# Optimization experiments

Hardware: AMD Instinct MI355X
Metric: run time of the kernel (lower is better)

Reference implementation:

```python
import jax, jax.numpy as jnp
import numpy as np

ALPHA = 0.6
K = 4


def gsdnef_conv(x, edge_index, W, b, alpha, K):
    """SpGSDNEFConv: linear transform then K-step graph-signal-denoising diffusion
    h_{k+1} = (x + alpha * A_hat h_k) / (1 + alpha), A_hat = D^-1/2 (A+I) D^-1/2."""
    n = x.shape[0]
    x = x @ W + b  # [N, C_out]
    loop = jnp.arange(n, dtype=edge_index.dtype)
    src = jnp.concatenate([edge_index[0], loop])
    dst = jnp.concatenate([edge_index[1], loop])
    ones = jnp.ones(src.shape, dtype=x.dtype)
    deg = jax.ops.segment_sum(ones, dst, num_segments=n)
    dinv = jax.lax.rsqrt(jnp.maximum(deg, 1e-12))
    norm = dinv[src] * dinv[dst]  # [E+N]
    inv = 1.0 / (1.0 + alpha)
    h = x
    for _ in range(K):
        agg = jax.ops.segment_sum(h[src] * norm[:, None], dst, num_segments=n)
        h = (x + alpha * agg) * inv
    return h


def setup_inputs() -> dict:
    key = jax.random.key(0)
    ks = jax.random.split(key, 16)
    N, E, C_in, H, C_out = 50000, 800000, 256, 128, 64
    x = jax.random.normal(ks[0], (N, C_in), dtype=jnp.float32)
    edge_index = jax.random.randint(ks[1], (2, E), 0, N, dtype=jnp.int64)

    def lin(k, fan_in, fan_out):
        k1, k2 = jax.random.split(k)
        bound = 1.0 / np.sqrt(fan_in)
        W = jax.random.uniform(k1, (fan_in, fan_out), jnp.float32, -bound, bound)
        b = jax.random.uniform(k2, (fan_out,), jnp.float32, -bound, bound)
        return W, b

    Wc1, bc1 = lin(ks[2], C_in, H)
    Wl1, bl1 = lin(ks[3], C_in, H)
    Wc2, bc2 = lin(ks[4], H, H)
    Wl2, bl2 = lin(ks[5], H, H)
    Wc3, bc3 = lin(ks[6], H, C_out)
    Wl3, bl3 = lin(ks[7], H, C_out)
    return dict(x=x, edge_index=edge_index,
                Wc1=Wc1, bc1=bc1, Wl1=Wl1, bl1=bl1,
                Wc2=Wc2, bc2=bc2, Wl2=Wl2, bl2=bl2,
                Wc3=Wc3, bc3=bc3, Wl3=Wl3, bl3=bl3)


def reference(x, edge_index, Wc1, bc1, Wl1, bl1, Wc2, bc2, Wl2, bl2, Wc3, bc3, Wl3, bl3):
    h = jax.nn.elu(gsdnef_conv(x, edge_index, Wc1, bc1, ALPHA, K) + (x @ Wl1 + bl1))
    h = jax.nn.elu(gsdnef_conv(h, edge_index, Wc2, bc2, ALPHA, K) + (h @ Wl2 + bl2))
    h = gsdnef_conv(h, edge_index, Wc3, bc3, ALPHA, K) + (h @ Wl3 + bl3)
    return h
```

## Files before the change

### kernel.cpp

```cpp
#include <hip/hip_runtime.h>
#include <hip/hip_fp16.h>
#include <math.h>

#define ALPHA_C 0.6f

typedef _Float16 f16;
typedef f16 f16x8 __attribute__((ext_vector_type(8)));
typedef float f32x4 __attribute__((ext_vector_type(4)));

__global__ void detect_idx_kernel(const void* __restrict__ ei, int* __restrict__ flag,
                                  int E, int N) {
    int i = blockIdx.x * blockDim.x + threadIdx.x;
    if (i >= E) return;
    long long v = ((const long long*)ei)[i];
    if (v < 0 || v >= (long long)N) *flag = 1;
}

__global__ void convert_idx_kernel(const void* __restrict__ ei, const int* __restrict__ flag,
                                   int* __restrict__ out, int n2e) {
    int i = blockIdx.x * blockDim.x + threadIdx.x;
    if (i >= n2e) return;
    if (*flag == 0)
        out[i] = (int)((const long long*)ei)[i];
    else
        out[i] = ((const int*)ei)[i];
}

__global__ void count_kernel(const int* __restrict__ dst, int* __restrict__ cnt, int E) {
    int i = blockIdx.x * blockDim.x + threadIdx.x;
    if (i < E) atomicAdd(&cnt[dst[i]], 1);
}

__global__ void dinv_kernel(const int* __restrict__ cnt, float* __restrict__ dinv, int N) {
    int i = blockIdx.x * blockDim.x + threadIdx.x;
    if (i < N) dinv[i] = rsqrtf((float)cnt[i] + 1.0f);
}

__global__ void block_reduce_kernel(const int* __restrict__ cnt, int* __restrict__ bsum, int n) {
    __shared__ int s[256];
    int tid = threadIdx.x;
    int i = blockIdx.x * 256 + tid;
    int v = (i < n) ? cnt[i] : 0;
    s[tid] = v;
    __syncthreads();
    for (int o = 128; o > 0; o >>= 1) {
        if (tid < o) s[tid] += s[tid + o];
        __syncthreads();
    }
    if (tid == 0) bsum[blockIdx.x] = s[0];
}

__global__ void scan_top_kernel(int* __restrict__ bsum, int nb) {
    __shared__ int s[1024];
    int tid = threadIdx.x;
    int v = (tid < nb) ? bsum[tid] : 0;
    s[tid] = v;
    __syncthreads();
    for (int o = 1; o < 1024; o <<= 1) {
        int t = (tid >= o) ? s[tid - o] : 0;
        __syncthreads();
        s[tid] += t;
        __syncthreads();
    }
    if (tid < nb) bsum[tid] = s[tid] - v;
}

__global__ void scan_fill_kernel(const int* __restrict__ cnt, const int* __restrict__ bsum,
                                 int* __restrict__ row_off, int n) {
    __shared__ int s[256];
    int tid = threadIdx.x;
    int i = blockIdx.x * 256 + tid;
    int v = (i < n) ? cnt[i] : 0;
    s[tid] = v;
    __syncthreads();
    for (int o = 1; o < 256; o <<= 1) {
        int t = (tid >= o) ? s[tid - o] : 0;
        __syncthreads();
        s[tid] += t;
        __syncthreads();
    }
    int base = bsum[blockIdx.x];
    if (i < n) row_off[i] = base + s[tid] - v;
    if (i == n - 1) row_off[n] = base + s[tid];
}

__global__ void fill_kernel(const int* __restrict__ src, const int* __restrict__ dst,
                            const float* __restrict__ dinv, const int* __restrict__ row_off,
                            int* __restrict__ cursor, unsigned int* __restrict__ csre, int E) {
    int e = blockIdx.x * blockDim.x + threadIdx.x;
    if (e >= E) return;
    int d = dst[e], s = src[e];
    int pos = atomicAdd(&cursor[d], 1);
    int idx = row_off[d] + pos;
    float w = dinv[s] * dinv[d];
    csre[idx] = (unsigned int)s |
                ((unsigned int)__half_as_ushort(__float2half(w)) << 16);
}

__global__ void prep_all_w_kernel(
    const float* __restrict__ Wc1, const float* __restrict__ Wl1,
    const float* __restrict__ Wc2, const float* __restrict__ Wl2,
    const float* __restrict__ Wc3, const float* __restrict__ Wl3,
    f16* __restrict__ w1c, f16* __restrict__ w1l,
    f16* __restrict__ w2c, f16* __restrict__ w2l,
    f16* __restrict__ w3c, f16* __restrict__ w3l) {
    int i = blockIdx.x * blockDim.x + threadIdx.x;
    const float* W; f16* O; int K, Nn, base;
    if      (i <  32768) { W = Wc1; O = w1c; K = 256; Nn = 128; base = i; }
    else if (i <  65536) { W = Wl1; O = w1l; K = 256; Nn = 128; base = i - 32768; }
    else if (i <  81920) { W = Wc2; O = w2c; K = 128; Nn = 128; base = i - 65536; }
    else if (i <  98304) { W = Wl2; O = w2l; K = 128; Nn = 128; base = i - 81920; }
    else if (i < 106496) { W = Wc3; O = w3c; K = 128; Nn = 64;  base = i - 98304; }
    else if (i < 114688) { W = Wl3; O = w3l; K = 128; Nn = 64;  base = i - 106496; }
    else return;
    int k = base / Nn, n = base - k * Nn;
    O[(size_t)n * K + k] = (f16)W[base];
}

template <int K, int NH, int AMODE>
__global__ __launch_bounds__(256) void gemm2_kernel(
    const void* __restrict__ A0v, const void* __restrict__ A1v,
    const f16* __restrict__ WtA, const f16* __restrict__ WtB,
    const float* __restrict__ biasA, const float* __restrict__ biasB,
    f16* __restrict__ CA, f16* __restrict__ CB, int M) {
    constexpr int BM = 64, BK = 64;
    constexpr int NT = 2 * NH / 16;
    constexpr int LDA = BK + 8;
    __shared__ f16 At[BM][LDA];
    __shared__ f16 Wt[2 * NH][LDA];

    int tid = threadIdx.x;
    int wave = tid >> 6, lane = tid & 63;
    int lr = lane & 15, lhi = lane >> 4;
    int m0 = blockIdx.x * BM;

    f32x4 acc[NT];
#pragma unroll
    for (int n = 0; n < NT; ++n) acc[n] = (f32x4){0.f, 0.f, 0.f, 0.f};

    for (int k0 = 0; k0 < K; k0 += BK) {
        for (int c = tid; c < BM * 8; c += 256) {
            int row = c >> 3, kc = (c & 7) << 3;
            f16x8 v;
#pragma unroll
            for (int j = 0; j < 8; ++j) v[j] = (f16)0.f;
            if (m0 + row < M) {
                size_t idx = (size_t)(m0 + row) * K + k0 + kc;
                if constexpr (AMODE == 0) {
                    v = *(const f16x8*)((const f16*)A0v + idx);
                } else if constexpr (AMODE == 1) {
                    float4 a = *(const float4*)((const float*)A0v + idx);
                    float4 b = *(const float4*)((const float*)A0v + idx + 4);
                    v[0] = (f16)a.x; v[1] = (f16)a.y; v[2] = (f16)a.z; v[3] = (f16)a.w;
                    v[4] = (f16)b.x; v[5] = (f16)b.y; v[6] = (f16)b.z; v[7] = (f16)b.w;
                } else {
                    f16x8 u0 = *(const f16x8*)((const f16*)A0v + idx);
                    f16x8 u1 = *(const f16x8*)((const f16*)A1v + idx);
#pragma unroll
                    for (int j = 0; j < 8; ++j) {
                        float t = (float)u0[j] + (float)u1[j];
                        v[j] = (f16)(t > 0.f ? t : expm1f(t));
                    }
                }
            }
            *(f16x8*)&At[row][kc] = v;
        }
        for (int c = tid; c < NH * 8; c += 256) {
            int row = c >> 3, kc = (c & 7) << 3;
            *(f16x8*)&Wt[row][kc]      = *(const f16x8*)(WtA + (size_t)row * K + k0 + kc);
            *(f16x8*)&Wt[NH + row][kc] = *(const f16x8*)(WtB + (size_t)row * K + k0 + kc);
        }
        __syncthreads();
#pragma unroll
        for (int kk = 0; kk < BK; kk += 32) {
            f16x8 a = *(const f16x8*)&At[wave * 16 + lr][kk + lhi * 8];
#pragma unroll
            for (int n = 0; n < NT; ++n) {
                f16x8 b = *(const f16x8*)&Wt[n * 16 + lr][kk + lhi * 8];
                acc[n] = __builtin_amdgcn_mfma_f32_16x16x32_f16(a, b, acc[n], 0, 0, 0);
            }
        }
        __syncthreads();
    }

    int rbase = m0 + wave * 16 + lhi * 4;
#pragma unroll
    for (int n = 0; n < NT; ++n) {
        bool isA = (n < NT / 2);
        int colg = (isA ? n : n - NT / 2) * 16 + lr;
        f16* outp = isA ? CA : CB;
        float bv = (isA ? biasA : biasB)[colg];
#pragma unroll
        for (int r = 0; r < 4; ++r) {
            int row = rbase + r;
            if (row < M) outp[(size_t)row * NH + colg] = (f16)(acc[n][r] + bv);
        }
    }
}

template <int C, bool FINAL>
__global__ __launch_bounds__(256) void diffuse16_kernel(
    const __half* __restrict__ h, const __half* __restrict__ xc,
    const float* __restrict__ dinv, const int* __restrict__ row_off,
    const unsigned int* __restrict__ csre, __half* __restrict__ hout,
    const f16* __restrict__ lin, float* __restrict__ fout, int N) {
    const float inv = 1.0f / (1.0f + ALPHA_C);
    int gid = blockIdx.x * blockDim.x + threadIdx.x;
    int node = gid >> 6;
    if (node >= N) return;
    int lane = threadIdx.x & 63;
    int l = lane & 15, grp = lane >> 4;
    float di = dinv[node];
    float di2 = di * di;
    int e0 = row_off[node], e1 = row_off[node + 1];

    if constexpr (C == 128) {
        float acc[8];
#pragma unroll
        for (int i = 0; i < 8; ++i) acc[i] = 0.f;
        size_t coff = (size_t)l * 8;

        if (grp == 0) {
            float4 rv = *(const float4*)(h + ((size_t)node << 7) + coff);
            const __half2* p = (const __half2*)&rv;
#pragma unroll
            for (int k = 0; k < 4; ++k) {
                float2 f = __half22float2(p[k]);
                acc[2 * k] += di2 * f.x;
                acc[2 * k + 1] += di2 * f.y;
            }
        }
        int e = e0 + grp;
        for (; e + 12 < e1; e += 16) {
            unsigned int ev0 = csre[e], ev1 = csre[e + 4], ev2 = csre[e + 8], ev3 = csre[e + 12];
            float4 r0 = *(const float4*)(h + ((size_t)(ev0 & 0xFFFF) << 7) + coff);
            float4 r1 = *(const float4*)(h + ((size_t)(ev1 & 0xFFFF) << 7) + coff);
            float4 r2 = *(const float4*)(h + ((size_t)(ev2 & 0xFFFF) << 7) + coff);
            float4 r3 = *(const float4*)(h + ((size_t)(ev3 & 0xFFFF) << 7) + coff);
            float w0 = __half2float(__ushort_as_half((unsigned short)(ev0 >> 16)));
            float w1 = __half2float(__ushort_as_half((unsigned short)(ev1 >> 16)));
            float w2 = __half2float(__ushort_as_half((unsigned short)(ev2 >> 16)));
            float w3 = __half2float(__ushort_as_half((unsigned short)(ev3 >> 16)));
            const __half2* p0 = (const __half2*)&r0;
            const __half2* p1 = (const __half2*)&r1;
            const __half2* p2 = (const __half2*)&r2;
            const __half2* p3 = (const __half2*)&r3;
#pragma unroll
            for (int k = 0; k < 4; ++k) {
                float2 f0 = __half22float2(p0[k]);
                float2 f1 = __half22float2(p1[k]);
                float2 f2 = __half22float2(p2[k]);
                float2 f3 = __half22float2(p3[k]);
                acc[2 * k]     += w0 * f0.x + w1 * f1.x + w2 * f2.x + w3 * f3.x;
                acc[2 * k + 1] += w0 * f0.y + w1 * f1.y + w2 * f2.y + w3 * f3.y;
            }
        }
        for (; e < e1; e += 4) {
            unsigned int ev0 = csre[e];
            float4 r0 = *(const float4*)(h + ((size_t)(ev0 & 0xFFFF) << 7) + coff);
            float w0 = __half2float(__ushort_as_half((unsigned short)(ev0 >> 16)));
            const __half2* p0 = (const __half2*)&r0;
#pragma unroll
            for (int k = 0; k < 4; ++k) {
                float2 f0 = __half22float2(p0[k]);
                acc[2 * k]     += w0 * f0.x;
                acc[2 * k + 1] += w0 * f0.y;
            }
        }
#pragma unroll
        for (int i = 0; i < 8; ++i) {
            acc[i] += __shfl_xor(acc[i], 16);
            acc[i] += __shfl_xor(acc[i], 32);
        }
        if (grp == 0) {
            float4 xv = *(const float4*)(xc + ((size_t)node << 7) + coff);
            const __half2* xp = (const __half2*)&xv;
            __half ov[8];
#pragma unroll
            for (int k = 0; k < 4; ++k) {
                float2 xf = __half22float2(xp[k]);
                ov[2 * k]     = __float2half((xf.x + ALPHA_C * acc[2 * k]) * inv);
                ov[2 * k + 1] = __float2half((xf.y + ALPHA_C * acc[2 * k + 1]) * inv);
            }
            *(float4*)(hout + ((size_t)node << 7) + coff) = *(float4*)ov;
        }
    } else {
        float acc[4];
#pragma unroll
        for (int i = 0; i < 4; ++i) acc[i] = 0.f;
        size_t coff = (size_t)l * 4;

        if (grp == 0) {
            float2 rv = *(const float2*)(h + ((size_t)node << 6) + coff);
            const __half2* p = (const __half2*)&rv;
#pragma unroll
            for (int k = 0; k < 2; ++k) {
                float2 f = __half22float2(p[k]);
                acc[2 * k] += di2 * f.x;
                acc[2 * k + 1] += di2 * f.y;
            }
        }
        int e = e0 + grp;
        for (; e + 12 < e1; e += 16) {
            unsigned int ev0 = csre[e], ev1 = csre[e + 4], ev2 = csre[e + 8], ev3 = csre[e + 12];
            float2 r0 = *(const float2*)(h + ((size_t)(ev0 & 0xFFFF) << 6) + coff);
            float2 r1 = *(const float2*)(h + ((size_t)(ev1 & 0xFFFF) << 6) + coff);
            float2 r2 = *(const float2*)(h + ((size_t)(ev2 & 0xFFFF) << 6) + coff);
            float2 r3 = *(const float2*)(h + ((size_t)(ev3 & 0xFFFF) << 6) + coff);
            float w0 = __half2float(__ushort_as_half((unsigned short)(ev0 >> 16)));
            float w1 = __half2float(__ushort_as_half((unsigned short)(ev1 >> 16)));
            float w2 = __half2float(__ushort_as_half((unsigned short)(ev2 >> 16)));
            float w3 = __half2float(__ushort_as_half((unsigned short)(ev3 >> 16)));
            const __half2* p0 = (const __half2*)&r0;
            const __half2* p1 = (const __half2*)&r1;
            const __half2* p2 = (const __half2*)&r2;
            const __half2* p3 = (const __half2*)&r3;
#pragma unroll
            for (int k = 0; k < 2; ++k) {
                float2 f0 = __half22float2(p0[k]);
                float2 f1 = __half22float2(p1[k]);
                float2 f2 = __half22float2(p2[k]);
                float2 f3 = __half22float2(p3[k]);
                acc[2 * k]     += w0 * f0.x + w1 * f1.x + w2 * f2.x + w3 * f3.x;
                acc[2 * k + 1] += w0 * f0.y + w1 * f1.y + w2 * f2.y + w3 * f3.y;
            }
        }
        for (; e < e1; e += 4) {
            unsigned int ev0 = csre[e];
            float2 r0 = *(const float2*)(h + ((size_t)(ev0 & 0xFFFF) << 6) + coff);
            float w0 = __half2float(__ushort_as_half((unsigned short)(ev0 >> 16)));
            const __half2* p0 = (const __half2*)&r0;
#pragma unroll
            for (int k = 0; k < 2; ++k) {
                float2 f0 = __half22float2(p0[k]);
                acc[2 * k]     += w0 * f0.x;
                acc[2 * k + 1] += w0 * f0.y;
            }
        }
#pragma unroll
        for (int i = 0; i < 4; ++i) {
            acc[i] += __shfl_xor(acc[i], 16);
            acc[i] += __shfl_xor(acc[i], 32);
        }
        if (grp == 0) {
            float2 xv = *(const float2*)(xc + ((size_t)node << 6) + coff);
            const __half2* xp = (const __half2*)&xv;
            float r[4];
#pragma unroll
            for (int k = 0; k < 2; ++k) {
                float2 xf = __half22float2(xp[k]);
                r[2 * k]     = (xf.x + ALPHA_C * acc[2 * k]) * inv;
                r[2 * k + 1] = (xf.y + ALPHA_C * acc[2 * k + 1]) * inv;
            }
            if constexpr (FINAL) {
                float2 lv = *(const float2*)(lin + ((size_t)node << 6) + coff);
                const __half2* lp = (const __half2*)&lv;
                float2 l0 = __half22float2(lp[0]);
                float2 l1 = __half22float2(lp[1]);
                float4 o;
                o.x = r[0] + l0.x; o.y = r[1] + l0.y;
                o.z = r[2] + l1.x; o.w = r[3] + l1.y;
                *(float4*)(fout + ((size_t)node << 6) + coff) = o;
            } else {
                __half ov[4];
#pragma unroll
                for (int k = 0; k < 4; ++k) ov[k] = __float2half(r[k]);
                *(float2*)(hout + ((size_t)node << 6) + coff) = *(float2*)ov;
            }
        }
    }
}

extern "C" void kernel_launch(void* const* d_in, const int* in_sizes, int n_in,
                              void* d_out, int out_size, void* d_ws, size_t ws_size,
                              hipStream_t stream) {
    const float* x   = (const float*)d_in[0];
    const void*  ei  = d_in[1];
    const float* Wc1 = (const float*)d_in[2];  const float* bc1 = (const float*)d_in[3];
    const float* Wl1 = (const float*)d_in[4];  const float* bl1 = (const float*)d_in[5];
    const float* Wc2 = (const float*)d_in[6];  const float* bc2 = (const float*)d_in[7];
    const float* Wl2 = (const float*)d_in[8];  const float* bl2 = (const float*)d_in[9];
    const float* Wc3 = (const float*)d_in[10]; const float* bc3 = (const float*)d_in[11];
    const float* Wl3 = (const float*)d_in[12]; const float* bl3 = (const float*)d_in[13];
    float* out = (float*)d_out;

    const int N = in_sizes[0] / 256;
    const int E = in_sizes[1] / 2;

    size_t off = 0;
    auto alloc = [&](size_t bytes) {
        void* p = (char*)d_ws + off;
        off += (bytes + 255) & ~(size_t)255;
        return p;
    };
    f16* B0 = (f16*)alloc((size_t)N * 128 * 2);
    f16* B1 = (f16*)alloc((size_t)N * 128 * 2);
    f16* B2 = (f16*)alloc((size_t)N * 128 * 2);
    f16* B3 = (f16*)alloc((size_t)N * 128 * 2);
    f16* B4 = (f16*)alloc((size_t)N * 128 * 2);
    f16* wt1c = (f16*)alloc((size_t)256 * 128 * 2);
    f16* wt1l = (f16*)alloc((size_t)256 * 128 * 2);
    f16* wt2c = (f16*)alloc((size_t)128 * 128 * 2);
    f16* wt2l = (f16*)alloc((size_t)128 * 128 * 2);
    f16* wt3c = (f16*)alloc((size_t)128 * 64 * 2);
    f16* wt3l = (f16*)alloc((size_t)128 * 64 * 2);
    float* dinv   = (float*)alloc((size_t)N * 4);
    int*   cnt    = (int*)  alloc((size_t)N * 4);
    int*   rowoff = (int*)  alloc((size_t)(N + 1) * 4);
    int*   bsum   = (int*)  alloc(1024 * 4);
    unsigned int* csre = (unsigned int*)alloc((size_t)E * 4);
    int*   idx32  = (int*)  alloc((size_t)2 * E * 4);
    int*   flag   = (int*)  alloc(4);
    int* src32 = idx32;
    int* dst32 = idx32 + E;

    const int TB = 256;
    int ge  = (E + TB - 1) / TB;
    int g2e = (2 * E + TB - 1) / TB;
    int gn  = (N + TB - 1) / TB;
    int nb  = (N + 255) / 256;

    hipMemsetAsync(flag, 0, 4, stream);
    detect_idx_kernel<<<ge, TB, 0, stream>>>(ei, flag, E, N);
    convert_idx_kernel<<<g2e, TB, 0, stream>>>(ei, flag, idx32, 2 * E);

    hipMemsetAsync(cnt, 0, (size_t)N * 4, stream);
    count_kernel<<<ge, TB, 0, stream>>>(dst32, cnt, E);
    dinv_kernel<<<gn, TB, 0, stream>>>(cnt, dinv, N);
    block_reduce_kernel<<<nb, 256, 0, stream>>>(cnt, bsum, N);
    scan_top_kernel<<<1, 1024, 0, stream>>>(bsum, nb);
    scan_fill_kernel<<<nb, 256, 0, stream>>>(cnt, bsum, rowoff, N);
    hipMemsetAsync(cnt, 0, (size_t)N * 4, stream);
    fill_kernel<<<ge, TB, 0, stream>>>(src32, dst32, dinv, rowoff, cnt, csre, E);

    prep_all_w_kernel<<<(114688 + TB - 1) / TB, TB, 0, stream>>>(
        Wc1, Wl1, Wc2, Wl2, Wc3, Wl3, wt1c, wt1l, wt2c, wt2l, wt3c, wt3l);

    int gm = (N + 63) / 64;
    int gd = (N * 64 + TB - 1) / TB;

    gemm2_kernel<256, 128, 1><<<gm, TB, 0, stream>>>(x, nullptr, wt1c, wt1l, bc1, bl1, B0, B1, N);
    diffuse16_kernel<128, false><<<gd, TB, 0, stream>>>((__half*)B0, (__half*)B0, dinv, rowoff, csre, (__half*)B2, nullptr, nullptr, N);
    diffuse16_kernel<128, false><<<gd, TB, 0, stream>>>((__half*)B2, (__half*)B0, dinv, rowoff, csre, (__half*)B3, nullptr, nullptr, N);
    diffuse16_kernel<128, false><<<gd, TB, 0, stream>>>((__half*)B3, (__half*)B0, dinv, rowoff, csre, (__half*)B2, nullptr, nullptr, N);
    diffuse16_kernel<128, false><<<gd, TB, 0, stream>>>((__half*)B2, (__half*)B0, dinv, rowoff, csre, (__half*)B3, nullptr, nullptr, N);

    gemm2_kernel<128, 128, 2><<<gm, TB, 0, stream>>>(B3, B1, wt2c, wt2l, bc2, bl2, B0, B4, N);
    diffuse16_kernel<128, false><<<gd, TB, 0, stream>>>((__half*)B0, (__half*)B0, dinv, rowoff, csre, (__half*)B1, nullptr, nullptr, N);
    diffuse16_kernel<128, false><<<gd, TB, 0, stream>>>((__half*)B1, (__half*)B0, dinv, rowoff, csre, (__half*)B2, nullptr, nullptr, N);
    diffuse16_kernel<128, false><<<gd, TB, 0, stream>>>((__half*)B2, (__half*)B0, dinv, rowoff, csre, (__half*)B1, nullptr, nullptr, N);
    diffuse16_kernel<128, false><<<gd, TB, 0, stream>>>((__half*)B1, (__half*)B0, dinv, rowoff, csre, (__half*)B2, nullptr, nullptr, N);

    gemm2_kernel<128, 64, 2><<<gm, TB, 0, stream>>>(B2, B4, wt3c, wt3l, bc3, bl3, B0, B1, N);
    diffuse16_kernel<64, false><<<gd, TB, 0, stream>>>((__half*)B0, (__half*)B0, dinv, rowoff, csre, (__half*)B2, nullptr, nullptr, N);
    diffuse16_kernel<64, false><<<gd, TB, 0, stream>>>((__half*)B2, (__half*)B0, dinv, rowoff, csre, (__half*)B3, nullptr, nullptr, N);
    diffuse16_kernel<64, false><<<gd, TB, 0, stream>>>((__half*)B3, (__half*)B0, dinv, rowoff, csre, (__half*)B2, nullptr, nullptr, N);
    diffuse16_kernel<64, true ><<<gd, TB, 0, stream>>>((__half*)B2, (__half*)B0, dinv, rowoff, csre, nullptr, B1, out, N);
}
```

Baseline: 577.0 us.

## Fuse index conversion with degree count, drop LDS in GEMM, widen C=64 diffusion loads

Index conversion and degree counting now run in one kernel, which removes a launch and a re-read of the destination array. The GEMM no longer stages tiles in shared memory: each wave loads its A fragments and weight fragments straight from global memory into MFMA operands, so the barriers and LDS traffic are gone but weights are reloaded redundantly per wave. The 64-channel diffusion kernel now uses 8 lanes × 8 halves per row, giving 16-byte gathers across 8 edge groups. That shortens the per-edge unroll and adds one extra shuffle stage.

New measurement: 626.8 us. 1.09x slower.

```diff
diff --git a/kernel.cpp b/kernel.cpp
--- a/kernel.cpp
+++ b/kernel.cpp
@@ -16,19 +16,18 @@
     if (v < 0 || v >= (long long)N) *flag = 1;
 }
 
-__global__ void convert_idx_kernel(const void* __restrict__ ei, const int* __restrict__ flag,
-                                   int* __restrict__ out, int n2e) {
+__global__ void convert_count_kernel(const void* __restrict__ ei, const int* __restrict__ flag,
+                                     int* __restrict__ out, int* __restrict__ cnt,
+                                     int E, int n2e) {
     int i = blockIdx.x * blockDim.x + threadIdx.x;
     if (i >= n2e) return;
+    int v;
     if (*flag == 0)
-        out[i] = (int)((const long long*)ei)[i];
+        v = (int)((const long long*)ei)[i];
     else
-        out[i] = ((const int*)ei)[i];
-}
-
-__global__ void count_kernel(const int* __restrict__ dst, int* __restrict__ cnt, int E) {
-    int i = blockIdx.x * blockDim.x + threadIdx.x;
-    if (i < E) atomicAdd(&cnt[dst[i]], 1);
+        v = ((const int*)ei)[i];
+    out[i] = v;
+    if (i >= E) atomicAdd(&cnt[v], 1);
 }
 
 __global__ void dinv_kernel(const int* __restrict__ cnt, float* __restrict__ dinv, int N) {
@@ -123,64 +122,50 @@
     const f16* __restrict__ WtA, const f16* __restrict__ WtB,
     const float* __restrict__ biasA, const float* __restrict__ biasB,
     f16* __restrict__ CA, f16* __restrict__ CB, int M) {
-    constexpr int BM = 64, BK = 64;
     constexpr int NT = 2 * NH / 16;
-    constexpr int LDA = BK + 8;
-    __shared__ f16 At[BM][LDA];
-    __shared__ f16 Wt[2 * NH][LDA];
-
     int tid = threadIdx.x;
     int wave = tid >> 6, lane = tid & 63;
     int lr = lane & 15, lhi = lane >> 4;
-    int m0 = blockIdx.x * BM;
+    int m0 = blockIdx.x * 64;
+
+    int arow = m0 + wave * 16 + lr;
+    int arow_c = arow < M ? arow : (M - 1);
 
     f32x4 acc[NT];
 #pragma unroll
     for (int n = 0; n < NT; ++n) acc[n] = (f32x4){0.f, 0.f, 0.f, 0.f};
 
-    for (int k0 = 0; k0 < K; k0 += BK) {
-        for (int c = tid; c < BM * 8; c += 256) {
-            int row = c >> 3, kc = (c & 7) << 3;
-            f16x8 v;
-#pragma unroll
-            for (int j = 0; j < 8; ++j) v[j] = (f16)0.f;
-            if (m0 + row < M) {
-                size_t idx = (size_t)(m0 + row) * K + k0 + kc;
-                if constexpr (AMODE == 0) {
-                    v = *(const f16x8*)((const f16*)A0v + idx);
-                } else if constexpr (AMODE == 1) {
-                    float4 a = *(const float4*)((const float*)A0v + idx);
-                    float4 b = *(const float4*)((const float*)A0v + idx + 4);
-                    v[0] = (f16)a.x; v[1] = (f16)a.y; v[2] = (f16)a.z; v[3] = (f16)a.w;
-                    v[4] = (f16)b.x; v[5] = (f16)b.y; v[6] = (f16)b.z; v[7] = (f16)b.w;
-                } else {
-                    f16x8 u0 = *(const f16x8*)((const f16*)A0v + idx);
-                    f16x8 u1 = *(const f16x8*)((const f16*)A1v + idx);
-#pragma unroll
-                    for (int j = 0; j < 8; ++j) {
-                        float t = (float)u0[j] + (float)u1[j];
-                        v[j] = (f16)(t > 0.f ? t : expm1f(t));
-                    }
-                }
-            }
-            *(f16x8*)&At[row][kc] = v;
-        }
-        for (int c = tid; c < NH * 8; c += 256) {
-            int row = c >> 3, kc = (c & 7) << 3;
-            *(f16x8*)&Wt[row][kc]      = *(const f16x8*)(WtA + (size_t)row * K + k0 + kc);
-            *(f16x8*)&Wt[NH + row][kc] = *(const f16x8*)(WtB + (size_t)row * K + k0 + kc);
-        }
-        __syncthreads();
-#pragma unroll
-        for (int kk = 0; kk < BK; kk += 32) {
-            f16x8 a = *(const f16x8*)&At[wave * 16 + lr][kk + lhi * 8];
-#pragma unroll
-            for (int n = 0; n < NT; ++n) {
-                f16x8 b = *(const f16x8*)&Wt[n * 16 + lr][kk + lhi * 8];
-                acc[n] = __builtin_amdgcn_mfma_f32_16x16x32_f16(a, b, acc[n], 0, 0, 0);
-            }
-        }
-        __syncthreads();
+    size_t aoff = (size_t)arow_c * K + lhi * 8;
+    size_t woff = (size_t)lr * K + lhi * 8;
+
+#pragma unroll 2
+    for (int ks = 0; ks < K; ks += 32) {
+        f16x8 a;
+        if constexpr (AMODE == 0) {
+            a = *(const f16x8*)((const f16*)A0v + aoff + ks);
+        } else if constexpr (AMODE == 1) {
+            const float* xp = (const float*)A0v + aoff + ks;
+            float4 a0 = *(const float4*)xp;
+            float4 a1 = *(const float4*)(xp + 4);
+            a[0] = (f16)a0.x; a[1] = (f16)a0.y; a[2] = (f16)a0.z; a[3] = (f16)a0.w;
+            a[4] = (f16)a1.x; a[5] = (f16)a1.y; a[6] = (f16)a1.z; a[7] = (f16)a1.w;
+        } else {
+            f16x8 u0 = *(const f16x8*)((const f16*)A0v + aoff + ks);
+            f16x8 u1 = *(const f16x8*)((const f16*)A1v + aoff + ks);
+#pragma unroll
+            for (int j = 0; j < 8; ++j) {
+                float t = (float)u0[j] + (float)u1[j];
+                a[j] = (f16)(t > 0.f ? t : expm1f(t));
+            }
+        }
+#pragma unroll
+        for (int n = 0; n < NT; ++n) {
+            const f16* wp = (n < NT / 2)
+                ? (WtA + (size_t)n * 16 * K)
+                : (WtB + (size_t)(n - NT / 2) * 16 * K);
+            f16x8 b = *(const f16x8*)(wp + woff + ks);
+            acc[n] = __builtin_amdgcn_mfma_f32_16x16x32_f16(a, b, acc[n], 0, 0, 0);
+        }
     }
 
     int rbase = m0 + wave * 16 + lhi * 4;
@@ -209,12 +194,12 @@
     int node = gid >> 6;
     if (node >= N) return;
     int lane = threadIdx.x & 63;
-    int l = lane & 15, grp = lane >> 4;
     float di = dinv[node];
     float di2 = di * di;
     int e0 = row_off[node], e1 = row_off[node + 1];
 
     if constexpr (C == 128) {
+        int l = lane & 15, grp = lane >> 4;
         float acc[8];
 #pragma unroll
         for (int i = 0; i < 8; ++i) acc[i] = 0.f;
@@ -285,87 +270,82 @@
             *(float4*)(hout + ((size_t)node << 7) + coff) = *(float4*)ov;
         }
     } else {
-        float acc[4];
-#pragma unroll
-        for (int i = 0; i < 4; ++i) acc[i] = 0.f;
-        size_t coff = (size_t)l * 4;
+        int l = lane & 7, grp = lane >> 3;
+        float acc[8];
+#pragma unroll
+        for (int i = 0; i < 8; ++i) acc[i] = 0.f;
+        size_t coff = (size_t)l * 8;
 
         if (grp == 0) {
-            float2 rv = *(const float2*)(h + ((size_t)node << 6) + coff);
+            float4 rv = *(const float4*)(h + ((size_t)node << 6) + coff);
             const __half2* p = (const __half2*)&rv;
 #pragma unroll
-            for (int k = 0; k < 2; ++k) {
+            for (int k = 0; k < 4; ++k) {
                 float2 f = __half22float2(p[k]);
                 acc[2 * k] += di2 * f.x;
                 acc[2 * k + 1] += di2 * f.y;
             }
         }
         int e = e0 + grp;
-        for (; e + 12 < e1; e += 16) {
-            unsigned int ev0 = csre[e], ev1 = csre[e + 4], ev2 = csre[e + 8], ev3 = csre[e + 12];
-            float2 r0 = *(const float2*)(h + ((size_t)(ev0 & 0xFFFF) << 6) + coff);
-            float2 r1 = *(const float2*)(h + ((size_t)(ev1 & 0xFFFF) << 6) + coff);
-            float2 r2 = *(const float2*)(h + ((size_t)(ev2 & 0xFFFF) << 6) + coff);
-            float2 r3 = *(const float2*)(h + ((size_t)(ev3 & 0xFFFF) << 6) + coff);
+        for (; e + 8 < e1; e += 16) {
+            unsigned int ev0 = csre[e], ev1 = csre[e + 8];
+            float4 r0 = *(const float4*)(h + ((size_t)(ev0 & 0xFFFF) << 6) + coff);
+            float4 r1 = *(const float4*)(h + ((size_t)(ev1 & 0xFFFF) << 6) + coff);
             float w0 = __half2float(__ushort_as_half((unsigned short)(ev0 >> 16)));
             float w1 = __half2float(__ushort_as_half((unsigned short)(ev1 >> 16)));
-            float w2 = __half2float(__ushort_as_half((unsigned short)(ev2 >> 16)));
-            float w3 = __half2float(__ushort_as_half((unsigned short)(ev3 >> 16)));
             const __half2* p0 = (const __half2*)&r0;
             const __half2* p1 = (const __half2*)&r1;
-            const __half2* p2 = (const __half2*)&r2;
-            const __half2* p3 = (const __half2*)&r3;
-#pragma unroll
-            for (int k = 0; k < 2; ++k) {
+#pragma unroll
+            for (int k = 0; k < 4; ++k) {
                 float2 f0 = __half22float2(p0[k]);
                 float2 f1 = __half22float2(p1[k]);
-                float2 f2 = __half22float2(p2[k]);
-                float2 f3 = __half22float2(p3[k]);
-                acc[2 * k]     += w0 * f0.x + w1 * f1.x + w2 * f2.x + w3 * f3.x;
-                acc[2 * k + 1] += w0 * f0.y + w1 * f1.y + w2 * f2.y + w3 * f3.y;
-            }
-        }
-        for (; e < e1; e += 4) {
+                acc[2 * k]     += w0 * f0.x + w1 * f1.x;
+                acc[2 * k + 1] += w0 * f0.y + w1 * f1.y;
+            }
+        }
+        if (e < e1) {
             unsigned int ev0 = csre[e];
-            float2 r0 = *(const float2*)(h + ((size_t)(ev0 & 0xFFFF) << 6) + coff);
+            float4 r0 = *(const float4*)(h + ((size_t)(ev0 & 0xFFFF) << 6) + coff);
             float w0 = __half2float(__ushort_as_half((unsigned short)(ev0 >> 16)));
             const __half2* p0 = (const __half2*)&r0;
 #pragma unroll
-            for (int k = 0; k < 2; ++k) {
+            for (int k = 0; k < 4; ++k) {
                 float2 f0 = __half22float2(p0[k]);
                 acc[2 * k]     += w0 * f0.x;
                 acc[2 * k + 1] += w0 * f0.y;
             }
         }
 #pragma unroll
-        for (int i = 0; i < 4; ++i) {
+        for (int i = 0; i < 8; ++i) {
+            acc[i] += __shfl_xor(acc[i], 8);
             acc[i] += __shfl_xor(acc[i], 16);
             acc[i] += __shfl_xor(acc[i], 32);
         }
         if (grp == 0) {
-            float2 xv = *(const float2*)(xc + ((size_t)node << 6) + coff);
+            float4 xv = *(const float4*)(xc + ((size_t)node << 6) + coff);
             const __half2* xp = (const __half2*)&xv;
-            float r[4];
-#pragma unroll
-            for (int k = 0; k < 2; ++k) {
+            float r[8];
+#pragma unroll
+            for (int k = 0; k < 4; ++k) {
                 float2 xf = __half22float2(xp[k]);
                 r[2 * k]     = (xf.x + ALPHA_C * acc[2 * k]) * inv;
                 r[2 * k + 1] = (xf.y + ALPHA_C * acc[2 * k + 1]) * inv;
             }
             if constexpr (FINAL) {
-                float2 lv = *(const float2*)(lin + ((size_t)node << 6) + coff);
-                const __half2* lp = (const __half2*)&lv;
-                float2 l0 = __half22float2(lp[0]);
-                float2 l1 = __half22float2(lp[1]);
-                float4 o;
-                o.x = r[0] + l0.x; o.y = r[1] + l0.y;
-                o.z = r[2] + l1.x; o.w = r[3] + l1.y;
-                *(float4*)(fout + ((size_t)node << 6) + coff) = o;
+                f16x8 lv = *(const f16x8*)(lin + ((size_t)node << 6) + coff);
+                float4 o0, o1;
+                o0.x = r[0] + (float)lv[0]; o0.y = r[1] + (float)lv[1];
+                o0.z = r[2] + (float)lv[2]; o0.w = r[3] + (float)lv[3];
+                o1.x = r[4] + (float)lv[4]; o1.y = r[5] + (float)lv[5];
+                o1.z = r[6] + (float)lv[6]; o1.w = r[7] + (float)lv[7];
+                float* op = fout + ((size_t)node << 6) + coff;
+                *(float4*)op = o0;
+                *(float4*)(op + 4) = o1;
             } else {
-                __half ov[4];
-#pragma unroll
-                for (int k = 0; k < 4; ++k) ov[k] = __float2half(r[k]);
-                *(float2*)(hout + ((size_t)node << 6) + coff) = *(float2*)ov;
+                __half ov[8];
+#pragma unroll
+                for (int k = 0; k < 8; ++k) ov[k] = __float2half(r[k]);
+                *(float4*)(hout + ((size_t)node << 6) + coff) = *(float4*)ov;
             }
         }
     }
@@ -421,11 +401,10 @@
     int nb  = (N + 255) / 256;
 
     hipMemsetAsync(flag, 0, 4, stream);
+    hipMemsetAsync(cnt, 0, (size_t)N * 4, stream);
     detect_idx_kernel<<<ge, TB, 0, stream>>>(ei, flag, E, N);
-    convert_idx_kernel<<<g2e, TB, 0, stream>>>(ei, flag, idx32, 2 * E);
-
-    hipMemsetAsync(cnt, 0, (size_t)N * 4, stream);
-    count_kernel<<<ge, TB, 0, stream>>>(dst32, cnt, E);
+    convert_count_kernel<<<g2e, TB, 0, stream>>>(ei, flag, idx32, cnt, E, 2 * E);
+
     dinv_kernel<<<gn, TB, 0, stream>>>(cnt, dinv, N);
     block_reduce_kernel<<<nb, 256, 0, stream>>>(cnt, bsum, N);
     scan_top_kernel<<<1, 1024, 0, stream>>>(bsum, nb);
```
